# Optimization experiments

Measured on AMD Instinct MI355X. Metric: run time of the kernel, lower is better.

Reference implementation:

```python
import jax, jax.numpy as jnp
import numpy as np

DIM = 768
NUM_HEADS = 12
HEAD_DIM = DIM // NUM_HEADS


def setup_inputs() -> dict:
    key = jax.random.key(0)
    ks = jax.random.split(key, 5)
    scale = 1.0 / np.sqrt(DIM)
    x = jax.random.normal(ks[0], (2, 2048, DIM), dtype=jnp.float32)
    W_qkv = jax.random.normal(ks[1], (DIM, 3 * DIM), dtype=jnp.float32) * scale
    b_qkv = jax.random.normal(ks[2], (3 * DIM,), dtype=jnp.float32) * 0.01
    W_proj = jax.random.normal(ks[3], (DIM, DIM), dtype=jnp.float32) * scale
    b_proj = jax.random.normal(ks[4], (DIM,), dtype=jnp.float32) * 0.01
    return {"x": x, "W_qkv": W_qkv, "b_qkv": b_qkv, "W_proj": W_proj, "b_proj": b_proj}


def reference(x, W_qkv, b_qkv, W_proj, b_proj):
    bsz, seqlen, dim = x.shape
    qkv = x @ W_qkv + b_qkv  # [b, s, 3*dim]
    q, k, v = jnp.split(qkv, 3, axis=-1)
    # [b, h, s, d]
    def split_heads(t):
        return t.reshape(bsz, seqlen, NUM_HEADS, HEAD_DIM).transpose(0, 2, 1, 3)
    q, k, v = split_heads(q), split_heads(k), split_heads(v)
    scores = jnp.einsum("bhqd,bhkd->bhqk", q, k) / np.sqrt(HEAD_DIM).astype(np.float32)
    causal = jnp.tril(jnp.ones((seqlen, seqlen), dtype=bool))
    scores = jnp.where(causal, scores, -jnp.inf)
    attn = jax.nn.softmax(scores, axis=-1)
    out = jnp.einsum("bhqk,bhkd->bhqd", attn, v)
    out = out.transpose(0, 2, 1, 3).reshape(bsz, seqlen, dim)
    return out @ W_proj + b_proj
```

## Files before the change

### kernel.cpp

```cpp
#include <hip/hip_runtime.h>

typedef __bf16 bf16;
typedef __bf16 bf16x8 __attribute__((ext_vector_type(8)));
typedef float f32x4 __attribute__((ext_vector_type(4)));

#define DIM 768
#define SEQ 2048
#define BATCH 2
#define NH 12
#define HD 64
#define M_TOT (BATCH*SEQ)
#define NQKV (3*DIM)
#define BK 32

__device__ __forceinline__ f32x4 mfma16(bf16x8 a, bf16x8 b, f32x4 c) {
    return __builtin_amdgcn_mfma_f32_16x16x32_bf16(a, b, c, 0, 0, 0);
}

template<int CTRL>
__device__ __forceinline__ float dppf(float x) {
    int xi = __builtin_bit_cast(int, x);
    int r = __builtin_amdgcn_update_dpp(0, xi, CTRL, 0xf, 0xf, true);
    return __builtin_bit_cast(float, r);
}
__device__ __forceinline__ float row16_sum(float v) {
    v += dppf<0xB1>(v);
    v += dppf<0x4E>(v);
    v += dppf<0x141>(v);
    v += dppf<0x140>(v);
    return v;
}

__device__ __forceinline__ void stage128x32(const bf16* g, int gstride, bf16* lds,
                                            int w, int lane) {
#pragma unroll
    for (int i = 0; i < 2; i++) {
        int p = (w*2 + i)*64 + lane;
        int r = p >> 2, c = p & 3;
        int s = c ^ ((r >> 1) & 3);
        __builtin_amdgcn_global_load_lds(
            (const __attribute__((address_space(1))) unsigned int*)(g + (size_t)r*gstride + s*8),
            (__attribute__((address_space(3))) unsigned int*)(lds + p*8),
            16, 0, 0);
    }
}
__device__ __forceinline__ bf16x8 frag128x32(const bf16* lds, int r, int quad) {
    int c = quad ^ ((r >> 1) & 3);
    return *(const bf16x8*)&lds[r*32 + c*8];
}

#define TQK_TILES ((DIM/32)*(NQKV/32))
#define TP_TILES  ((DIM/32)*(DIM/32))
#define CAST_BLOCKS 768
__global__ __launch_bounds__(256) void prep_kernel(
    const float* __restrict__ x, const float* __restrict__ Wqkv,
    const float* __restrict__ Wproj,
    bf16* __restrict__ xb, bf16* __restrict__ Wqt, bf16* __restrict__ Wpt)
{
    const int bid = blockIdx.x;
    if (bid < TQK_TILES + TP_TILES) {
        const float* src; bf16* dst; int NN, KK, t;
        if (bid < TQK_TILES) { src = Wqkv; dst = Wqt; NN = NQKV; KK = DIM; t = bid; }
        else                 { src = Wproj; dst = Wpt; NN = DIM;  KK = DIM; t = bid - TQK_TILES; }
        const int ntn = NN / 32;
        const int tk = t / ntn, tn = t - tk * ntn;
        __shared__ float tile[32][33];
        const int tx = threadIdx.x & 31, ty = threadIdx.x >> 5;
#pragma unroll
        for (int i = 0; i < 4; i++)
            tile[ty + i*8][tx] = src[(size_t)(tk*32 + ty + i*8)*NN + tn*32 + tx];
        __syncthreads();
#pragma unroll
        for (int i = 0; i < 4; i++)
            dst[(size_t)(tn*32 + ty + i*8)*KK + tk*32 + tx] = (bf16)tile[tx][ty + i*8];
    } else {
        const int b2 = bid - (TQK_TILES + TP_TILES);
        const int N4 = M_TOT*DIM/4;
        for (int i = b2*256 + (int)threadIdx.x; i < N4; i += CAST_BLOCKS*256) {
            float4 v = ((const float4*)x)[i];
            bf16 o[4] = {(bf16)v.x, (bf16)v.y, (bf16)v.z, (bf16)v.w};
            *(uint2*)&xb[(size_t)i*4] = *(uint2*)o;
        }
    }
}

__global__ __launch_bounds__(256) void qkv_gemm(
    const bf16* __restrict__ A,
    const bf16* __restrict__ Bt,
    const float* __restrict__ bias,
    bf16* __restrict__ qkv)
{
    __shared__ bf16 As[128*32];
    __shared__ bf16 Bs[128*32];
    const int K = DIM;
    const int tid = threadIdx.x;
    const int row0 = blockIdx.y * 128, col0 = blockIdx.x * 128;
    const int w = tid >> 6, lane = tid & 63, quad = lane >> 4, l16 = lane & 15;
    const int wy = w >> 1, wx = w & 1;

    f32x4 acc[4][4];
#pragma unroll
    for (int mi = 0; mi < 4; mi++)
#pragma unroll
        for (int ni = 0; ni < 4; ni++)
            acc[mi][ni] = (f32x4){0.f,0.f,0.f,0.f};

    for (int k0 = 0; k0 < K; k0 += BK) {
        __syncthreads();
        stage128x32(A  + (size_t)row0*K + k0, K, As, w, lane);
        stage128x32(Bt + (size_t)col0*K + k0, K, Bs, w, lane);
        __syncthreads();
        bf16x8 af[4], bfv[4];
#pragma unroll
        for (int mi = 0; mi < 4; mi++)
            af[mi] = frag128x32(As, wy*64 + mi*16 + l16, quad);
#pragma unroll
        for (int ni = 0; ni < 4; ni++)
            bfv[ni] = frag128x32(Bs, wx*64 + ni*16 + l16, quad);
#pragma unroll
        for (int mi = 0; mi < 4; mi++)
#pragma unroll
            for (int ni = 0; ni < 4; ni++)
                acc[mi][ni] = mfma16(af[mi], bfv[ni], acc[mi][ni]);
    }

    const int which = col0 / DIM;
    if (which < 2) {
#pragma unroll
        for (int mi = 0; mi < 4; mi++)
#pragma unroll
            for (int ni = 0; ni < 4; ni++)
#pragma unroll
                for (int rr = 0; rr < 4; rr++) {
                    int r = row0 + wy*64 + mi*16 + quad*4 + rr;
                    int c = col0 + wx*64 + ni*16 + l16;
                    float v = acc[mi][ni][rr] + bias[c];
                    int cc = c - which*DIM;
                    int h = cc >> 6, d = cc & 63;
                    int bb = r >> 11, sq = r & (SEQ-1);
                    size_t idx = ((((size_t)which*BATCH + bb)*NH + h)*SEQ + sq)*HD + d;
                    qkv[idx] = (bf16)v;
                }
    } else {
        bf16* Vg = qkv + (size_t)2*BATCH*NH*SEQ*HD;
#pragma unroll
        for (int mi = 0; mi < 4; mi++) {
            int r = row0 + wy*64 + mi*16 + quad*4;
            int bb = r >> 11, sq = r & (SEQ-1);
#pragma unroll
            for (int ni = 0; ni < 4; ni++) {
                int c = col0 + wx*64 + ni*16 + l16;
                int cc = c - 2*DIM;
                int h = cc >> 6, d = cc & 63;
                float bv = bias[c];
                bf16 tmp[4];
#pragma unroll
                for (int rr = 0; rr < 4; rr++)
                    tmp[rr] = (bf16)(acc[mi][ni][rr] + bv);
                size_t idx = (((size_t)bb*NH + h)*HD + d)*SEQ + sq;
                *(uint2*)&Vg[idx] = *(uint2*)tmp;
            }
        }
    }
}

#define ALD 72
__global__ __launch_bounds__(256) void attn_kernel(
    const bf16* __restrict__ Q,
    const bf16* __restrict__ Kb,
    const bf16* __restrict__ Vb,
    bf16* __restrict__ attnout,
    bf16* __restrict__ Opart,
    float* __restrict__ lpart)
{
    const int chunk = blockIdx.x;
    const int qt = 31 - (int)blockIdx.y;
    const int bh = blockIdx.z;
    const int b = bh / NH, h = bh - b*NH;

    int kt0, kt1;
    if (qt < 16) { if (chunk) return; kt0 = 0; kt1 = qt; }
    else if (chunk == 0) { kt0 = 0; kt1 = 15; }
    else { kt0 = 16; kt1 = qt; }

    __shared__ bf16 Kt[64*ALD];
    __shared__ bf16 Vt[64*ALD];
    __shared__ bf16 Pl[4][16*ALD];

    const int tid = threadIdx.x, w = tid >> 6, lane = tid & 63;
    const int quad = lane >> 4, l16 = lane & 15;

    const size_t hoff = ((size_t)bh)*SEQ*HD;
    const bf16* Qh = Q + hoff;
    const bf16* Kh = Kb + hoff;
    const bf16* Vh = Vb + hoff;

    const int qrow0 = qt*64 + w*16;
    bf16x8 qf[2];
#pragma unroll
    for (int ks = 0; ks < 2; ks++)
        qf[ks] = *(const bf16x8*)&Qh[(size_t)(qrow0 + l16)*HD + ks*32 + quad*8];

    f32x4 of[4];
#pragma unroll
    for (int i = 0; i < 4; i++) of[i] = (f32x4){0.f,0.f,0.f,0.f};
    float lrow[4] = {0.f, 0.f, 0.f, 0.f};

    const float SCL = 0.125f * 1.44269504088896f;

    for (int kt = kt0; kt <= kt1; kt++) {
        __syncthreads();
#pragma unroll
        for (int i = 0; i < 2; i++) {
            int idx = tid + i*256;
            int r = idx >> 3, seg = idx & 7;
            *(uint4*)&Kt[r*ALD + seg*8] = *(const uint4*)&Kh[(size_t)(kt*64 + r)*HD + seg*8];
        }
#pragma unroll
        for (int i = 0; i < 2; i++) {
            int idx = tid + i*256;
            int r = idx >> 3, seg = idx & 7;
            *(uint4*)&Vt[r*ALD + seg*8] = *(const uint4*)&Vh[(size_t)r*SEQ + kt*64 + seg*8];
        }
        __syncthreads();

        f32x4 sf[4];
#pragma unroll
        for (int nt = 0; nt < 4; nt++) sf[nt] = (f32x4){0.f,0.f,0.f,0.f};
#pragma unroll
        for (int nt = 0; nt < 4; nt++)
#pragma unroll
            for (int ks = 0; ks < 2; ks++) {
                bf16x8 kfv = *(const bf16x8*)&Kt[(nt*16 + l16)*ALD + ks*32 + quad*8];
                sf[nt] = mfma16(qf[ks], kfv, sf[nt]);
            }

        const bool diag = (kt == qt);
        bf16* pl = &Pl[w][0];
#pragma unroll
        for (int rr = 0; rr < 4; rr++) {
            int qg = qt*64 + w*16 + quad*4 + rr;
            float ps = 0.f;
#pragma unroll
            for (int nt = 0; nt < 4; nt++) {
                float s = sf[nt][rr] * SCL;
                if (diag && (kt*64 + nt*16 + l16) > qg) s = -1e30f;
                float p = exp2f(s);
                ps += p;
                pl[(quad*4 + rr)*ALD + nt*16 + l16] = (bf16)p;
            }
            lrow[rr] += ps;
        }

#pragma unroll
        for (int ks2 = 0; ks2 < 2; ks2++) {
            bf16x8 pa = *(const bf16x8*)&pl[l16*ALD + ks2*32 + quad*8];
#pragma unroll
            for (int nt2 = 0; nt2 < 4; nt2++) {
                bf16x8 vv = *(const bf16x8*)&Vt[(nt2*16 + l16)*ALD + ks2*32 + quad*8];
                of[nt2] = mfma16(pa, vv, of[nt2]);
            }
        }
    }

#pragma unroll
    for (int rr = 0; rr < 4; rr++) lrow[rr] = row16_sum(lrow[rr]);

    if (qt < 16) {
#pragma unroll
        for (int rr = 0; rr < 4; rr++) {
            float inv = 1.0f / lrow[rr];
            int g = b*SEQ + qt*64 + w*16 + quad*4 + rr;
#pragma unroll
            for (int nt2 = 0; nt2 < 4; nt2++)
                attnout[(size_t)g*DIM + h*HD + nt2*16 + l16] = (bf16)(of[nt2][rr] * inv);
        }
    } else {
        size_t slot = ((size_t)bh*16 + (qt - 16))*2 + chunk;
        bf16* Os = Opart + slot*4096;
        float* ls = lpart + slot*64;
#pragma unroll
        for (int rr = 0; rr < 4; rr++) {
            int row = w*16 + quad*4 + rr;
            if (l16 == 0) ls[row] = lrow[rr];
#pragma unroll
            for (int nt2 = 0; nt2 < 4; nt2++)
                Os[(size_t)row*64 + nt2*16 + l16] = (bf16)of[nt2][rr];
        }
    }
}

__global__ __launch_bounds__(256) void merge_kernel(
    const bf16* __restrict__ Opart, const float* __restrict__ lpart,
    bf16* __restrict__ attnout)
{
    const int qi = blockIdx.x;
    const int bh = blockIdx.y;
    const int b = bh / NH, h = bh - b*NH;
    const int t = threadIdx.x;
    const int row = t >> 2, cs = t & 3;

    size_t slot0 = ((size_t)bh*16 + qi)*2;
    const bf16* O0 = Opart + slot0*4096 + (size_t)row*64 + cs*16;
    const bf16* O1 = O0 + 4096;
    float inv = 1.0f / (lpart[slot0*64 + row] + lpart[(slot0+1)*64 + row]);

    bf16x8 a0 = *(const bf16x8*)O0;
    bf16x8 a1 = *(const bf16x8*)(O0 + 8);
    bf16x8 b0 = *(const bf16x8*)O1;
    bf16x8 b1 = *(const bf16x8*)(O1 + 8);
    bf16 outv[16];
#pragma unroll
    for (int j = 0; j < 8; j++) {
        outv[j]     = (bf16)(((float)a0[j] + (float)b0[j]) * inv);
        outv[8 + j] = (bf16)(((float)a1[j] + (float)b1[j]) * inv);
    }
    size_t o = ((size_t)b*SEQ + (16 + qi)*64 + row)*DIM + h*HD + cs*16;
    *(uint4*)&attnout[o]     = *(uint4*)&outv[0];
    *(uint4*)&attnout[o + 8] = *(uint4*)&outv[8];
}

__global__ __launch_bounds__(256) void proj_gemm(
    const bf16* __restrict__ A,
    const bf16* __restrict__ Bt,
    const float* __restrict__ bias,
    float* __restrict__ out)
{
    __shared__ bf16 As[128*32];
    __shared__ bf16 Bs[128*32];
    const int K = DIM;
    const int tid = threadIdx.x;
    const int row0 = blockIdx.y * 128, col0 = blockIdx.x * 128;
    const int w = tid >> 6, lane = tid & 63, quad = lane >> 4, l16 = lane & 15;
    const int wy = w >> 1, wx = w & 1;

    f32x4 acc[4][4];
#pragma unroll
    for (int mi = 0; mi < 4; mi++)
#pragma unroll
        for (int ni = 0; ni < 4; ni++)
            acc[mi][ni] = (f32x4){0.f,0.f,0.f,0.f};

    for (int k0 = 0; k0 < K; k0 += BK) {
        __syncthreads();
        stage128x32(A  + (size_t)row0*K + k0, K, As, w, lane);
        stage128x32(Bt + (size_t)col0*K + k0, K, Bs, w, lane);
        __syncthreads();
        bf16x8 af[4], bfv[4];
#pragma unroll
        for (int mi = 0; mi < 4; mi++)
            af[mi] = frag128x32(As, wy*64 + mi*16 + l16, quad);
#pragma unroll
        for (int ni = 0; ni < 4; ni++)
            bfv[ni] = frag128x32(Bs, wx*64 + ni*16 + l16, quad);
#pragma unroll
        for (int mi = 0; mi < 4; mi++)
#pragma unroll
            for (int ni = 0; ni < 4; ni++)
                acc[mi][ni] = mfma16(af[mi], bfv[ni], acc[mi][ni]);
    }

#pragma unroll
    for (int mi = 0; mi < 4; mi++)
#pragma unroll
        for (int ni = 0; ni < 4; ni++)
#pragma unroll
            for (int rr = 0; rr < 4; rr++) {
                int r = row0 + wy*64 + mi*16 + quad*4 + rr;
                int c = col0 + wx*64 + ni*16 + l16;
                out[(size_t)r*DIM + c] = acc[mi][ni][rr] + bias[c];
            }
}

extern "C" void kernel_launch(void* const* d_in, const int* in_sizes, int n_in,
                              void* d_out, int out_size, void* d_ws, size_t ws_size,
                              hipStream_t stream) {
    const float* x     = (const float*)d_in[0];
    const float* Wqkv  = (const float*)d_in[1];
    const float* bqkv  = (const float*)d_in[2];
    const float* Wproj = (const float*)d_in[3];
    const float* bproj = (const float*)d_in[4];
    float* out = (float*)d_out;

    bf16* xb   = (bf16*)d_ws;
    bf16* Wqt  = xb  + (size_t)M_TOT*DIM;
    bf16* Wpt  = Wqt + (size_t)NQKV*DIM;
    bf16* qkvb = Wpt + (size_t)DIM*DIM;
    bf16* attn = qkvb + (size_t)3*M_TOT*DIM;

    bf16*  Opart = xb;
    float* lpart = (float*)Wqt;

    const size_t headsz = (size_t)BATCH*NH*SEQ*HD;

    prep_kernel<<<TQK_TILES + TP_TILES + CAST_BLOCKS, 256, 0, stream>>>(
        x, Wqkv, Wproj, xb, Wqt, Wpt);
    qkv_gemm<<<dim3(NQKV/128, M_TOT/128), 256, 0, stream>>>(xb, Wqt, bqkv, qkvb);
    attn_kernel<<<dim3(2, SEQ/64, BATCH*NH), 256, 0, stream>>>(
        qkvb, qkvb + headsz, qkvb + 2*headsz, attn, Opart, lpart);
    merge_kernel<<<dim3(16, BATCH*NH), 256, 0, stream>>>(Opart, lpart, attn);
    proj_gemm<<<dim3(DIM/128, M_TOT/128), 256, 0, stream>>>(attn, Wpt, bproj, out);
}
```

Baseline: 202.4 us.

## Rebalance attention KV split, prefetch K/V tiles in registers, swizzle LDS

Changes the split-KV scheme so every query tile at or above index 8 is split into two balanced halves instead of only tiles 16 and up, which evens out per-block work. K/V tiles for the next iteration are prefetched into registers while the current tile is computed. LDS padding is replaced with an XOR swizzle, and the QK MFMA operand order is swapped so each lane owns a query row, letting the row sum be reduced with two shuffles instead of DPP. Workspace layout and the merge kernel change to match, at the cost of more partial buffers and extra merge work.

```diff
diff --git a/kernel.cpp b/kernel.cpp
--- a/kernel.cpp
+++ b/kernel.cpp
@@ -15,20 +15,6 @@
 
 __device__ __forceinline__ f32x4 mfma16(bf16x8 a, bf16x8 b, f32x4 c) {
     return __builtin_amdgcn_mfma_f32_16x16x32_bf16(a, b, c, 0, 0, 0);
-}
-
-template<int CTRL>
-__device__ __forceinline__ float dppf(float x) {
-    int xi = __builtin_bit_cast(int, x);
-    int r = __builtin_amdgcn_update_dpp(0, xi, CTRL, 0xf, 0xf, true);
-    return __builtin_bit_cast(float, r);
-}
-__device__ __forceinline__ float row16_sum(float v) {
-    v += dppf<0xB1>(v);
-    v += dppf<0x4E>(v);
-    v += dppf<0x141>(v);
-    v += dppf<0x140>(v);
-    return v;
 }
 
 __device__ __forceinline__ void stage128x32(const bf16* g, int gstride, bf16* lds,
@@ -164,8 +150,7 @@
     }
 }
 
-#define ALD 72
-__global__ __launch_bounds__(256) void attn_kernel(
+__global__ __launch_bounds__(256, 6) void attn_kernel(
     const bf16* __restrict__ Q,
     const bf16* __restrict__ Kb,
     const bf16* __restrict__ Vb,
@@ -179,18 +164,21 @@
     const int b = bh / NH, h = bh - b*NH;
 
     int kt0, kt1;
-    if (qt < 16) { if (chunk) return; kt0 = 0; kt1 = qt; }
-    else if (chunk == 0) { kt0 = 0; kt1 = 15; }
-    else { kt0 = 16; kt1 = qt; }
-
-    __shared__ bf16 Kt[64*ALD];
-    __shared__ bf16 Vt[64*ALD];
-    __shared__ bf16 Pl[4][16*ALD];
+    if (qt < 8) { if (chunk) return; kt0 = 0; kt1 = qt; }
+    else {
+        int hh = (qt + 1) >> 1;
+        if (chunk == 0) { kt0 = 0; kt1 = hh - 1; }
+        else            { kt0 = hh; kt1 = qt; }
+    }
+
+    __shared__ bf16 Kt[64*64];
+    __shared__ bf16 Vt[64*64];
+    __shared__ bf16 Pl[4][16*72];
 
     const int tid = threadIdx.x, w = tid >> 6, lane = tid & 63;
     const int quad = lane >> 4, l16 = lane & 15;
 
-    const size_t hoff = ((size_t)bh)*SEQ*HD;
+    const size_t hoff = (size_t)bh*SEQ*HD;
     const bf16* Qh = Q + hoff;
     const bf16* Kh = Kb + hoff;
     const bf16* Vh = Vb + hoff;
@@ -204,88 +192,108 @@
     f32x4 of[4];
 #pragma unroll
     for (int i = 0; i < 4; i++) of[i] = (f32x4){0.f,0.f,0.f,0.f};
-    float lrow[4] = {0.f, 0.f, 0.f, 0.f};
+    float lsum = 0.f;
+
+    const int p0 = w*128 + lane;
+    const int r0 = p0 >> 3, s0 = (p0 & 7) ^ (r0 & 7);
+    const int p1 = p0 + 64;
+    const int r1 = p1 >> 3, s1 = (p1 & 7) ^ (r1 & 7);
+
+    uint4 kpre[2], vpre[2];
+    {
+        kpre[0] = *(const uint4*)&Kh[(size_t)(kt0*64 + r0)*HD + s0*8];
+        kpre[1] = *(const uint4*)&Kh[(size_t)(kt0*64 + r1)*HD + s1*8];
+        vpre[0] = *(const uint4*)&Vh[(size_t)r0*SEQ + kt0*64 + s0*8];
+        vpre[1] = *(const uint4*)&Vh[(size_t)r1*SEQ + kt0*64 + s1*8];
+    }
 
     const float SCL = 0.125f * 1.44269504088896f;
+    bf16* pl = &Pl[w][0];
 
     for (int kt = kt0; kt <= kt1; kt++) {
         __syncthreads();
-#pragma unroll
-        for (int i = 0; i < 2; i++) {
-            int idx = tid + i*256;
-            int r = idx >> 3, seg = idx & 7;
-            *(uint4*)&Kt[r*ALD + seg*8] = *(const uint4*)&Kh[(size_t)(kt*64 + r)*HD + seg*8];
-        }
-#pragma unroll
-        for (int i = 0; i < 2; i++) {
-            int idx = tid + i*256;
-            int r = idx >> 3, seg = idx & 7;
-            *(uint4*)&Vt[r*ALD + seg*8] = *(const uint4*)&Vh[(size_t)r*SEQ + kt*64 + seg*8];
-        }
-        __syncthreads();
+        *(uint4*)&Kt[p0*8] = kpre[0];
+        *(uint4*)&Kt[p1*8] = kpre[1];
+        *(uint4*)&Vt[p0*8] = vpre[0];
+        *(uint4*)&Vt[p1*8] = vpre[1];
+        __syncthreads();
+
+        if (kt < kt1) {
+            kpre[0] = *(const uint4*)&Kh[(size_t)((kt+1)*64 + r0)*HD + s0*8];
+            kpre[1] = *(const uint4*)&Kh[(size_t)((kt+1)*64 + r1)*HD + s1*8];
+            vpre[0] = *(const uint4*)&Vh[(size_t)r0*SEQ + (kt+1)*64 + s0*8];
+            vpre[1] = *(const uint4*)&Vh[(size_t)r1*SEQ + (kt+1)*64 + s1*8];
+        }
 
         f32x4 sf[4];
 #pragma unroll
         for (int nt = 0; nt < 4; nt++) sf[nt] = (f32x4){0.f,0.f,0.f,0.f};
 #pragma unroll
-        for (int nt = 0; nt < 4; nt++)
+        for (int nt = 0; nt < 4; nt++) {
+            int r = nt*16 + l16;
 #pragma unroll
             for (int ks = 0; ks < 2; ks++) {
-                bf16x8 kfv = *(const bf16x8*)&Kt[(nt*16 + l16)*ALD + ks*32 + quad*8];
-                sf[nt] = mfma16(qf[ks], kfv, sf[nt]);
+                bf16x8 kf = *(const bf16x8*)&Kt[r*64 + (((ks*4+quad) ^ (r&7))*8)];
+                sf[nt] = mfma16(kf, qf[ks], sf[nt]);
             }
+        }
 
         const bool diag = (kt == qt);
-        bf16* pl = &Pl[w][0];
+        const int qg = qt*64 + w*16 + l16;
+#pragma unroll
+        for (int nt = 0; nt < 4; nt++) {
+            bf16 t4[4];
+#pragma unroll
+            for (int rr = 0; rr < 4; rr++) {
+                float s = sf[nt][rr] * SCL;
+                if (diag && (kt*64 + nt*16 + quad*4 + rr) > qg) s = -1e30f;
+                float p = __builtin_amdgcn_exp2f(s);
+                lsum += p;
+                t4[rr] = (bf16)p;
+            }
+            *(uint2*)&pl[l16*72 + nt*16 + quad*4] = *(uint2*)t4;
+        }
+
+        bf16x8 pa[2];
+        pa[0] = *(const bf16x8*)&pl[l16*72 + quad*8];
+        pa[1] = *(const bf16x8*)&pl[l16*72 + 32 + quad*8];
+#pragma unroll
+        for (int dm = 0; dm < 4; dm++) {
+            int r = dm*16 + l16;
+#pragma unroll
+            for (int ks = 0; ks < 2; ks++) {
+                bf16x8 vv = *(const bf16x8*)&Vt[r*64 + (((ks*4+quad) ^ (r&7))*8)];
+                of[dm] = mfma16(pa[ks], vv, of[dm]);
+            }
+        }
+    }
+
+    lsum += __shfl_xor(lsum, 16);
+    lsum += __shfl_xor(lsum, 32);
+
+    if (qt < 8) {
+        float linv[4];
+#pragma unroll
+        for (int rr = 0; rr < 4; rr++)
+            linv[rr] = 1.0f / __shfl(lsum, quad*4 + rr);
 #pragma unroll
         for (int rr = 0; rr < 4; rr++) {
-            int qg = qt*64 + w*16 + quad*4 + rr;
-            float ps = 0.f;
-#pragma unroll
-            for (int nt = 0; nt < 4; nt++) {
-                float s = sf[nt][rr] * SCL;
-                if (diag && (kt*64 + nt*16 + l16) > qg) s = -1e30f;
-                float p = exp2f(s);
-                ps += p;
-                pl[(quad*4 + rr)*ALD + nt*16 + l16] = (bf16)p;
-            }
-            lrow[rr] += ps;
-        }
-
-#pragma unroll
-        for (int ks2 = 0; ks2 < 2; ks2++) {
-            bf16x8 pa = *(const bf16x8*)&pl[l16*ALD + ks2*32 + quad*8];
-#pragma unroll
-            for (int nt2 = 0; nt2 < 4; nt2++) {
-                bf16x8 vv = *(const bf16x8*)&Vt[(nt2*16 + l16)*ALD + ks2*32 + quad*8];
-                of[nt2] = mfma16(pa, vv, of[nt2]);
-            }
-        }
-    }
-
-#pragma unroll
-    for (int rr = 0; rr < 4; rr++) lrow[rr] = row16_sum(lrow[rr]);
-
-    if (qt < 16) {
-#pragma unroll
-        for (int rr = 0; rr < 4; rr++) {
-            float inv = 1.0f / lrow[rr];
             int g = b*SEQ + qt*64 + w*16 + quad*4 + rr;
 #pragma unroll
-            for (int nt2 = 0; nt2 < 4; nt2++)
-                attnout[(size_t)g*DIM + h*HD + nt2*16 + l16] = (bf16)(of[nt2][rr] * inv);
+            for (int dm = 0; dm < 4; dm++)
+                attnout[(size_t)g*DIM + h*HD + dm*16 + l16] = (bf16)(of[dm][rr] * linv[rr]);
         }
     } else {
-        size_t slot = ((size_t)bh*16 + (qt - 16))*2 + chunk;
+        size_t slot = ((size_t)bh*24 + (qt - 8))*2 + chunk;
         bf16* Os = Opart + slot*4096;
         float* ls = lpart + slot*64;
+        if (quad == 0) ls[w*16 + l16] = lsum;
 #pragma unroll
         for (int rr = 0; rr < 4; rr++) {
             int row = w*16 + quad*4 + rr;
-            if (l16 == 0) ls[row] = lrow[rr];
-#pragma unroll
-            for (int nt2 = 0; nt2 < 4; nt2++)
-                Os[(size_t)row*64 + nt2*16 + l16] = (bf16)of[nt2][rr];
+#pragma unroll
+            for (int dm = 0; dm < 4; dm++)
+                Os[(size_t)row*64 + dm*16 + l16] = (bf16)of[dm][rr];
         }
     }
 }
@@ -300,7 +308,7 @@
     const int t = threadIdx.x;
     const int row = t >> 2, cs = t & 3;
 
-    size_t slot0 = ((size_t)bh*16 + qi)*2;
+    size_t slot0 = ((size_t)bh*24 + qi)*2;
     const bf16* O0 = Opart + slot0*4096 + (size_t)row*64 + cs*16;
     const bf16* O1 = O0 + 4096;
     float inv = 1.0f / (lpart[slot0*64 + row] + lpart[(slot0+1)*64 + row]);
@@ -315,7 +323,7 @@
         outv[j]     = (bf16)(((float)a0[j] + (float)b0[j]) * inv);
         outv[8 + j] = (bf16)(((float)a1[j] + (float)b1[j]) * inv);
     }
-    size_t o = ((size_t)b*SEQ + (16 + qi)*64 + row)*DIM + h*HD + cs*16;
+    size_t o = ((size_t)b*SEQ + (8 + qi)*64 + row)*DIM + h*HD + cs*16;
     *(uint4*)&attnout[o]     = *(uint4*)&outv[0];
     *(uint4*)&attnout[o + 8] = *(uint4*)&outv[8];
 }
@@ -389,7 +397,7 @@
     bf16* attn = qkvb + (size_t)3*M_TOT*DIM;
 
     bf16*  Opart = xb;
-    float* lpart = (float*)Wqt;
+    float* lpart = (float*)(xb + (size_t)24*24*2*4096);
 
     const size_t headsz = (size_t)BATCH*NH*SEQ*HD;
 
@@ -398,6 +406,6 @@
     qkv_gemm<<<dim3(NQKV/128, M_TOT/128), 256, 0, stream>>>(xb, Wqt, bqkv, qkvb);
     attn_kernel<<<dim3(2, SEQ/64, BATCH*NH), 256, 0, stream>>>(
         qkvb, qkvb + headsz, qkvb + 2*headsz, attn, Opart, lpart);
-    merge_kernel<<<dim3(16, BATCH*NH), 256, 0, stream>>>(Opart, lpart, attn);
+    merge_kernel<<<dim3(24, BATCH*NH), 256, 0, stream>>>(Opart, lpart, attn);
     proj_gemm<<<dim3(DIM/128, M_TOT/128), 256, 0, stream>>>(attn, Wpt, bproj, out);
 }
```

Result: slower. 237.5 us (+17.4%).
